# Kernel optimization log

Measured on AMD Instinct MI355X. Metric: run time of the kernel, lower is better.

## Reference

```python
import jax, jax.numpy as jnp
import numpy as np

N_NODES = 50000
N_EDGES = 800000
N_GRAPHS = 512
HID = 128
N_LAYERS = 4
EPS = 1e-4


def setup_inputs() -> dict:
    key = jax.random.key(0)
    ks = jax.random.split(key, 20)
    s = 0.05
    return {
        "z": jax.random.randint(ks[0], (N_NODES,), 0, 100),
        "pos": jax.random.normal(ks[1], (N_NODES, 3), jnp.float32),
        "batch": jnp.sort(jax.random.randint(ks[2], (N_NODES,), 0, N_GRAPHS)),
        "edge_index": jax.random.randint(ks[3], (2, N_EDGES), 0, N_NODES),
        "embed_tab": jax.random.normal(ks[4], (100, HID), jnp.float32) * s,
        "W_pos": jax.random.normal(ks[5], (3, HID), jnp.float32) * s,
        "b_pos": jax.random.normal(ks[6], (HID,), jnp.float32) * s,
        "W_comb": jax.random.normal(ks[7], (2 * HID, HID), jnp.float32) * s,
        "b_comb": jax.random.normal(ks[8], (HID,), jnp.float32) * s,
        "gin_W1": jax.random.normal(ks[9], (N_LAYERS, HID, HID), jnp.float32) * s,
        "gin_b1": jax.random.normal(ks[10], (N_LAYERS, HID), jnp.float32) * s,
        "gin_W2": jax.random.normal(ks[11], (N_LAYERS, HID, HID), jnp.float32) * s,
        "gin_b2": jax.random.normal(ks[12], (N_LAYERS, HID), jnp.float32) * s,
        # heads stacked in order: [alpha, beta, nu, gamma]
        "head_W1": jax.random.normal(ks[13], (4, HID, HID), jnp.float32) * s,
        "head_b1": jax.random.normal(ks[14], (4, HID), jnp.float32) * s,
        "head_W2": jax.random.normal(ks[15], (4, HID, 1), jnp.float32) * s,
        "head_b2": jax.random.normal(ks[16], (4, 1), jnp.float32) * s,
    }


def _forward(z, pos, batch, edge_index, embed_tab, W_pos, b_pos, W_comb, b_comb,
             gin_W1, gin_b1, gin_W2, gin_b2, head_W1, head_b1, head_W2, head_b2):
    # initial embedding: atom embed + linear pos embed -> combine MLP
    atom = embed_tab[z]                                    # [N, H]
    pemb = pos @ W_pos + b_pos                             # [N, H]
    x = jax.nn.relu(jnp.concatenate([atom, pemb], -1) @ W_comb + b_comb)
    src, dst = edge_index[0], edge_index[1]
    # GIN stack: h = MLP(x + sum_{j in N(i)} x_j); ReLU between convs, none after last
    for l in range(N_LAYERS):
        agg = jax.ops.segment_sum(x[src], dst, num_segments=N_NODES)  # [N, H]
        h = x + agg                                        # eps = 0
        h = jax.nn.relu(h @ gin_W1[l] + gin_b1[l]) @ gin_W2[l] + gin_b2[l]
        x = jax.nn.relu(h) if l < N_LAYERS - 1 else h
    # sum pooling per graph
    aggr = jax.ops.segment_sum(x, batch, num_segments=N_GRAPHS)  # [G, F]
    # 4 heads (alpha, beta, nu, gamma), each Linear-ReLU-Linear -> [4, G, 1]
    hh = jax.nn.relu(jnp.einsum('gh,khf->kgf', aggr, head_W1) + head_b1[:, None, :])
    out = jnp.einsum('kgf,kfo->kgo', hh, head_W2) + head_b2[:, None, :]
    alpha = jnp.maximum(jax.nn.softplus(out[0]) + 1.0, 1.0 + EPS)
    beta = jax.nn.softplus(out[1])
    nu = jax.nn.softplus(out[2])
    gamma = out[3]
    aleatoric = beta / (alpha - 1.0)
    epistemic = beta / ((alpha - 1.0) * nu)
    return (gamma, aleatoric, epistemic, nu, alpha, beta)


def reference(z, pos, batch, edge_index, embed_tab, W_pos, b_pos, W_comb, b_comb,
              gin_W1, gin_b1, gin_W2, gin_b2, head_W1, head_b1, head_W2, head_b2):
    return _forward(z, pos, batch, edge_index, embed_tab, W_pos, b_pos, W_comb,
                    b_comb, gin_W1, gin_b1, gin_W2, gin_b2, head_W1, head_b1,
                    head_W2, head_b2)
```

## Files before the change

kernel.cpp:

```cpp
#include <hip/hip_runtime.h>
#include <stdint.h>

#define NN 50000
#define NE 800000
#define NG 512
#define H  128
#define NBK 196
#define EPB 3125

typedef __attribute__((ext_vector_type(8))) short short8;
typedef __attribute__((ext_vector_type(16))) float f32x16;

union U4S8 { uint4 u; short8 s; };

__device__ __forceinline__ float softplusf(float x){
    return fmaxf(x, 0.f) + log1pf(expf(-fabsf(x)));
}

__device__ __forceinline__ unsigned rne_bf16_hi(float x){
    unsigned u = __float_as_uint(x);
    unsigned r = u + 0x7fffu + ((u >> 16) & 1u);
    return r & 0xffff0000u;
}

__device__ __forceinline__ void split_pack(float x0, float x1, unsigned &hi, unsigned &lo){
    unsigned h0 = rne_bf16_hi(x0), h1 = rne_bf16_hi(x1);
    hi = (h0 >> 16) | h1;
    float l0 = x0 - __uint_as_float(h0);
    float l1 = x1 - __uint_as_float(h1);
    unsigned g0 = rne_bf16_hi(l0), g1 = rne_bf16_hi(l1);
    lo = (g0 >> 16) | g1;
}

__global__ void k_sentinel(float* out, float val){
    int i = blockIdx.x*256 + threadIdx.x;
    if (i < 6*NG) out[i] = val;
}

__global__ __launch_bounds__(64) void k_wsplit(const float* __restrict__ gW1,
    const float* __restrict__ gW2, uint4* __restrict__ wf)
{
    int bid = blockIdx.x, lane = threadIdx.x;
    int mat = bid >> 5, ntg = (bid >> 3) & 3, ks = bid & 7;
    int l = mat >> 1;
    const float* W = (mat & 1) ? (gW2 + (size_t)l*H*H) : (gW1 + (size_t)l*H*H);
    int n  = ntg*32 + (lane & 31);
    int kb = ks*16 + (lane >> 5)*8;
    unsigned hi[4], lo[4];
#pragma unroll
    for (int d=0; d<4; d++){
        float x0 = W[(size_t)(kb + 2*d    )*H + n];
        float x1 = W[(size_t)(kb + 2*d + 1)*H + n];
        split_pack(x0, x1, hi[d], lo[d]);
    }
    int bh = ((mat*2 + 0)*4 + ntg)*8 + ks;
    int bl = ((mat*2 + 1)*4 + ntg)*8 + ks;
    wf[bh*64 + lane] = make_uint4(hi[0],hi[1],hi[2],hi[3]);
    wf[bl*64 + lane] = make_uint4(lo[0],lo[1],lo[2],lo[3]);
}

__global__ __launch_bounds__(64) void k_wsplit_embed(const float* __restrict__ Wc,
    uint4* __restrict__ wcf)
{
    int bid = blockIdx.x, lane = threadIdx.x;
    int ntg = bid >> 4, ks = bid & 15;
    int n  = ntg*32 + (lane & 31);
    int kb = ks*16 + (lane >> 5)*8;
    unsigned hi[4], lo[4];
#pragma unroll
    for (int d=0; d<4; d++){
        float x0 = Wc[(size_t)(kb + 2*d    )*H + n];
        float x1 = Wc[(size_t)(kb + 2*d + 1)*H + n];
        split_pack(x0, x1, hi[d], lo[d]);
    }
    wcf[((0*4 + ntg)*16 + ks)*64 + lane] = make_uint4(hi[0],hi[1],hi[2],hi[3]);
    wcf[((1*4 + ntg)*16 + ks)*64 + lane] = make_uint4(lo[0],lo[1],lo[2],lo[3]);
}

__global__ __launch_bounds__(256) void k_embed_mfma(const int* __restrict__ z,
    const float* __restrict__ pos, const float* __restrict__ emb,
    const float* __restrict__ Wp, const float* __restrict__ bp,
    const float* __restrict__ bc, const uint4* __restrict__ wcf,
    unsigned* __restrict__ xbu)
{
    __shared__ unsigned short AhiF[2*8*64*8];
    __shared__ unsigned short AloF[2*8*64*8];
    const int t = threadIdx.x, lane = t & 63, w = t >> 6;
    const int rt = w & 1, cp = w >> 1;
    const int mb = blockIdx.x * 64;
    const int c31 = lane & 31;
    const int q = lane >> 5;

    const int r = t >> 2, c4 = t & 3;
    const int gr = mb + r;
    const int gre = (gr < NN) ? gr : (NN-1);
    const int zr = z[gre];
    const float p0 = pos[gre*3+0], p1 = pos[gre*3+1], p2 = pos[gre*3+2];
    const int rt_s = r >> 5, r31s = r & 31;

    f32x16 acc0, acc1;
#pragma unroll
    for (int i=0;i<16;i++){ acc0[i]=0.f; acc1[i]=0.f; }

#pragma unroll
    for (int kh2=0; kh2<2; kh2++){
        if (kh2) __syncthreads();
#pragma unroll
        for (int i=0;i<8;i++){
            int cl = c4*4 + i*16;
            float4 v;
            if (kh2 == 0){
                v = *(const float4*)(emb + (size_t)zr*H + cl);
            } else {
                float4 w0 = *(const float4*)(Wp + cl);
                float4 w1 = *(const float4*)(Wp + H + cl);
                float4 w2 = *(const float4*)(Wp + 2*H + cl);
                float4 bb = *(const float4*)(bp + cl);
                v.x = p0*w0.x + p1*w1.x + p2*w2.x + bb.x;
                v.y = p0*w0.y + p1*w1.y + p2*w2.y + bb.y;
                v.z = p0*w0.z + p1*w1.z + p2*w2.z + bb.z;
                v.w = p0*w0.w + p1*w1.w + p2*w2.w + bb.w;
            }
            unsigned h0,l0,h1,l1;
            split_pack(v.x, v.y, h0, l0);
            split_pack(v.z, v.w, h1, l1);
            int idx = ((rt_s*8 + (cl>>4))*64 + ((cl>>3)&1)*32 + r31s)*8 + (cl & 7);
            *(uint2*)&AhiF[idx] = make_uint2(h0, h1);
            *(uint2*)&AloF[idx] = make_uint2(l0, l1);
        }
        __syncthreads();
#pragma unroll
        for (int ks=0; ks<8; ks++){
            int ksg = kh2*8 + ks;
            U4S8 ah, al, bh0, bl0, bh1, bl1;
            ah.u  = *(const uint4*)&AhiF[((rt*8+ks)*64 + lane)*8];
            al.u  = *(const uint4*)&AloF[((rt*8+ks)*64 + lane)*8];
            bh0.u = wcf[((0*4 + 2*cp+0)*16 + ksg)*64 + lane];
            bl0.u = wcf[((1*4 + 2*cp+0)*16 + ksg)*64 + lane];
            bh1.u = wcf[((0*4 + 2*cp+1)*16 + ksg)*64 + lane];
            bl1.u = wcf[((1*4 + 2*cp+1)*16 + ksg)*64 + lane];
            acc0 = __builtin_amdgcn_mfma_f32_32x32x16_bf16(ah.s, bh0.s, acc0, 0,0,0);
            acc0 = __builtin_amdgcn_mfma_f32_32x32x16_bf16(ah.s, bl0.s, acc0, 0,0,0);
            acc0 = __builtin_amdgcn_mfma_f32_32x32x16_bf16(al.s, bh0.s, acc0, 0,0,0);
            acc1 = __builtin_amdgcn_mfma_f32_32x32x16_bf16(ah.s, bh1.s, acc1, 0,0,0);
            acc1 = __builtin_amdgcn_mfma_f32_32x32x16_bf16(ah.s, bl1.s, acc1, 0,0,0);
            acc1 = __builtin_amdgcn_mfma_f32_32x32x16_bf16(al.s, bh1.s, acc1, 0,0,0);
        }
    }

    const float bva = bc[64*cp + c31], bvb = bc[64*cp + 32 + c31];
#pragma unroll
    for (int reg=0; reg<16; reg++){
        int row = 32*rt + (reg & 3) + 8*(reg >> 2) + 4*q;
        int mm = mb + row;
        if (mm < NN){
            float v0 = fmaxf(acc0[reg] + bva, 0.f);
            float v1 = fmaxf(acc1[reg] + bvb, 0.f);
            float pa = __shfl_xor(v0, 1);
            float pb = __shfl_xor(v1, 1);
            if (!(lane & 1)){
                unsigned u0 = (rne_bf16_hi(v0) >> 16) | (rne_bf16_hi(pa) & 0xffff0000u);
                unsigned u1 = (rne_bf16_hi(v1) >> 16) | (rne_bf16_hi(pb) & 0xffff0000u);
                xbu[(size_t)mm*64 + 32*cp      + (c31>>1)] = u0;
                xbu[(size_t)mm*64 + 32*cp + 16 + (c31>>1)] = u1;
            }
        }
    }
}

__global__ __launch_bounds__(256) void k_gin_fused(
    const unsigned* __restrict__ xbin,
    const int* __restrict__ iptr, const int* __restrict__ esrc,
    const float* __restrict__ b1, const float* __restrict__ b2,
    const uint4* __restrict__ wf,
    float* __restrict__ xout, unsigned* __restrict__ xbout,
    int l, int relu2, int wx, int wxb)
{
    __shared__ unsigned short AhiF[8*64*8];
    __shared__ unsigned short AloF[8*64*8];
    __shared__ int eS[1024];
    const int t = threadIdx.x, lane = t & 63, w = t >> 6;
    const int mb = blockIdx.x * 32;
    const int c31 = lane & 31;
    const int q = lane >> 5;
    const int c  = lane & 15;
    const int jr = lane >> 4;
    const int ksw = c >> 1, qw = c & 1;

    const uint4* __restrict__ xbp = (const uint4*)xbin;

    const int eTop = (mb + 32 < NN) ? (mb + 32) : NN;
    int e0b = iptr[mb];
    int e1b = iptr[eTop];
    e0b = max(0, min(e0b, NE));
    e1b = max(e0b, min(e1b, NE));
    const int ecnt = e1b - e0b;
    for (int i = t; i < ecnt && i < 1024; i += 256) eS[i] = esrc[e0b + i];
    __syncthreads();
    const int eCap = e0b + 1024;
    const int* ixL = (const int*)eS - e0b;

#define ACC8(U)  { unsigned _u; \
    _u=(U).x; a0 += __uint_as_float(_u<<16); a1 += __uint_as_float(_u&0xffff0000u); \
    _u=(U).y; a2 += __uint_as_float(_u<<16); a3 += __uint_as_float(_u&0xffff0000u); \
    _u=(U).z; a4 += __uint_as_float(_u<<16); a5 += __uint_as_float(_u&0xffff0000u); \
    _u=(U).w; a6 += __uint_as_float(_u<<16); a7 += __uint_as_float(_u&0xffff0000u); }

#define GLOOP(IX) { \
    for (; j+8 <= e; j += 8){ \
        int i0=IX[j+0], i1=IX[j+1], i2=IX[j+2], i3=IX[j+3]; \
        int i4=IX[j+4], i5=IX[j+5], i6=IX[j+6], i7=IX[j+7]; \
        uint4 u0 = xbp[(size_t)i0*16 + c]; \
        uint4 u1 = xbp[(size_t)i1*16 + c]; \
        uint4 u2 = xbp[(size_t)i2*16 + c]; \
        uint4 u3 = xbp[(size_t)i3*16 + c]; \
        uint4 u4 = xbp[(size_t)i4*16 + c]; \
        uint4 u5 = xbp[(size_t)i5*16 + c]; \
        uint4 u6 = xbp[(size_t)i6*16 + c]; \
        uint4 u7 = xbp[(size_t)i7*16 + c]; \
        ACC8(u0); ACC8(u1); ACC8(u2); ACC8(u3); \
        ACC8(u4); ACC8(u5); ACC8(u6); ACC8(u7); \
    } \
    for (; j+2 <= e; j += 2){ \
        int i0=IX[j+0], i1=IX[j+1]; \
        uint4 u0 = xbp[(size_t)i0*16 + c]; \
        uint4 u1 = xbp[(size_t)i1*16 + c]; \
        ACC8(u0); ACC8(u1); \
    } \
    if (j < e){ \
        int i0=IX[j]; \
        uint4 u0 = xbp[(size_t)i0*16 + c]; \
        ACC8(u0); \
    } }

#pragma unroll
    for (int p=0; p<2; p++){
        int m  = w*8 + p*4 + jr;
        int mm = mb + m;
        int mme = (mm < NN) ? mm : (NN-1);
        int s = iptr[mme], e = iptr[mme+1];
        s = max(0, min(s, NE));
        e = max(s, min(e, NE));
        float a0=0.f,a1=0.f,a2=0.f,a3=0.f,a4=0.f,a5=0.f,a6=0.f,a7=0.f;
        {
            uint4 su = xbp[(size_t)mme*16 + c];
            ACC8(su);
        }
        int j = s;
        if (s >= e0b && e <= eCap){
            GLOOP(ixL);
        } else {
            GLOOP(esrc);
        }
        unsigned hi4x, hi4y, hi4z, hi4w, lo4x, lo4y, lo4z, lo4w;
        split_pack(a0, a1, hi4x, lo4x);
        split_pack(a2, a3, hi4y, lo4y);
        split_pack(a4, a5, hi4z, lo4z);
        split_pack(a6, a7, hi4w, lo4w);
        int idx = (ksw*64 + qw*32 + (m ^ ksw))*8;
        *(uint4*)&AhiF[idx] = make_uint4(hi4x, hi4y, hi4z, hi4w);
        *(uint4*)&AloF[idx] = make_uint4(lo4x, lo4y, lo4z, lo4w);
    }
#undef GLOOP
#undef ACC8
    __syncthreads();

    const float bv1 = b1[w*32 + c31];
    const float bv2 = b2[w*32 + c31];
    const int mat1 = l*2, mat2 = l*2 + 1;

    f32x16 acc;
#pragma unroll
    for (int i=0;i<16;i++) acc[i] = 0.f;

#pragma unroll
    for (int ks=0; ks<8; ks++){
        U4S8 ah, al, bh, bl;
        ah.u = *(const uint4*)&AhiF[(ks*64 + q*32 + (c31 ^ ks))*8];
        al.u = *(const uint4*)&AloF[(ks*64 + q*32 + (c31 ^ ks))*8];
        bh.u = wf[(((mat1*2+0)*4 + w)*8 + ks)*64 + lane];
        bl.u = wf[(((mat1*2+1)*4 + w)*8 + ks)*64 + lane];
        acc = __builtin_amdgcn_mfma_f32_32x32x16_bf16(ah.s, bh.s, acc, 0,0,0);
        acc = __builtin_amdgcn_mfma_f32_32x32x16_bf16(ah.s, bl.s, acc, 0,0,0);
        acc = __builtin_amdgcn_mfma_f32_32x32x16_bf16(al.s, bh.s, acc, 0,0,0);
    }

    __syncthreads();
    {
        int k   = w*32 + c31;
        int kst = k >> 4, qt = (k >> 3) & 1, jj = k & 7;
#pragma unroll
        for (int reg=0; reg<16; reg++){
            int row = (reg & 3) + 8*(reg >> 2) + 4*q;
            float v = fmaxf(acc[reg] + bv1, 0.f);
            int idx = (kst*64 + qt*32 + (row ^ kst))*8 + jj;
            unsigned hb = rne_bf16_hi(v);
            AhiF[idx] = (unsigned short)(hb >> 16);
            AloF[idx] = (unsigned short)(rne_bf16_hi(v - __uint_as_float(hb)) >> 16);
        }
    }
    __syncthreads();

#pragma unroll
    for (int i=0;i<16;i++) acc[i] = 0.f;
#pragma unroll
    for (int ks=0; ks<8; ks++){
        U4S8 ah, al, bh, bl;
        ah.u = *(const uint4*)&AhiF[(ks*64 + q*32 + (c31 ^ ks))*8];
        al.u = *(const uint4*)&AloF[(ks*64 + q*32 + (c31 ^ ks))*8];
        bh.u = wf[(((mat2*2+0)*4 + w)*8 + ks)*64 + lane];
        bl.u = wf[(((mat2*2+1)*4 + w)*8 + ks)*64 + lane];
        acc = __builtin_amdgcn_mfma_f32_32x32x16_bf16(ah.s, bh.s, acc, 0,0,0);
        acc = __builtin_amdgcn_mfma_f32_32x32x16_bf16(ah.s, bl.s, acc, 0,0,0);
        acc = __builtin_amdgcn_mfma_f32_32x32x16_bf16(al.s, bh.s, acc, 0,0,0);
    }

#pragma unroll
    for (int reg=0; reg<16; reg++){
        int row = (reg & 3) + 8*(reg >> 2) + 4*q;
        int mm = mb + row;
        if (mm < NN){
            float v = acc[reg] + bv2;
            if (relu2) v = fmaxf(v, 0.f);
            if (wx) xout[(size_t)mm*H + w*32 + c31] = v;
            if (wxb){
                float p = __shfl_xor(v, 1);
                if (!(lane & 1)){
                    unsigned u = (rne_bf16_hi(v) >> 16) | (rne_bf16_hi(p) & 0xffff0000u);
                    xbout[(size_t)mm*64 + w*16 + (c31>>1)] = u;
                }
            }
        }
    }
}

__global__ __launch_bounds__(256) void k_hist(const int* __restrict__ ei, int* __restrict__ cnt){
    __shared__ int hist[256];
    int blk = blockIdx.x, t = threadIdx.x;
    hist[t] = 0;
    __syncthreads();
    int e0 = blk*EPB, e1 = min(e0+EPB, NE);
    for (int e = e0+t; e < e1; e += 256){
        int d = ei[NE+e];
        if ((unsigned)d < NN) atomicAdd(&hist[d>>8], 1);
    }
    __syncthreads();
    if (t < NBK) cnt[t*256 + blk] = hist[t];
}

__global__ __launch_bounds__(256) void k_btot(const int* __restrict__ cnt, int* __restrict__ tot){
    __shared__ int s[256];
    int k = blockIdx.x, t = threadIdx.x;
    s[t] = cnt[k*256 + t];
    __syncthreads();
    for (int sd=128; sd>0; sd>>=1){
        if (t < sd) s[t] += s[t+sd];
        __syncthreads();
    }
    if (t == 0) tot[k] = s[0];
}

__global__ __launch_bounds__(256) void k_bscan(const int* __restrict__ tot, int* __restrict__ bb){
    __shared__ int sc[256];
    int t = threadIdx.x;
    int v = (t < NBK) ? tot[t] : 0;
    sc[t] = v;
    for (int off=1; off<256; off<<=1){
        __syncthreads();
        int tv = (t >= off) ? sc[t-off] : 0;
        __syncthreads();
        sc[t] += tv;
    }
    __syncthreads();
    if (t == 0) bb[0] = 0;
    if (t < NBK) bb[t+1] = sc[t];
}

__global__ __launch_bounds__(256) void k_soff(const int* __restrict__ cnt,
    const int* __restrict__ bb, int* __restrict__ soff)
{
    __shared__ int sc[256];
    int k = blockIdx.x, t = threadIdx.x;
    int v = cnt[k*256 + t];
    sc[t] = v;
    for (int off=1; off<256; off<<=1){
        __syncthreads();
        int tv = (t >= off) ? sc[t-off] : 0;
        __syncthreads();
        sc[t] += tv;
    }
    __syncthreads();
    soff[k*256 + t] = bb[k] + sc[t] - v;
}

__global__ __launch_bounds__(256) void k_part(const int* __restrict__ ei,
    const int* __restrict__ soff, unsigned* __restrict__ tmp)
{
    __shared__ unsigned edgeL[EPB];
    __shared__ int sc[256], startv[256], curv[256];
    __shared__ int tots;
    int blk = blockIdx.x, t = threadIdx.x;
    sc[t] = 0;
    __syncthreads();
    int e0 = blk*EPB, e1 = min(e0+EPB, NE);
    for (int e = e0+t; e < e1; e += 256){
        int d = ei[NE+e];
        if ((unsigned)d < NN) atomicAdd(&sc[d>>8], 1);
    }
    __syncthreads();
    int v = sc[t];
    for (int off=1; off<256; off<<=1){
        __syncthreads();
        int tv = (t >= off) ? sc[t-off] : 0;
        __syncthreads();
        sc[t] += tv;
    }
    __syncthreads();
    startv[t] = sc[t] - v;
    curv[t]   = sc[t] - v;
    if (t == 255) tots = sc[255];
    __syncthreads();
    for (int e = e0+t; e < e1; e += 256){
        int d = ei[NE+e];
        if ((unsigned)d < NN){
            unsigned u = (unsigned)ei[e] | ((unsigned)d << 16);
            int p = atomicAdd(&curv[d>>8], 1);
            edgeL[p] = u;
        }
    }
    __syncthreads();
    int nTot = tots;
    for (int i = t; i < nTot; i += 256){
        unsigned u = edgeL[i];
        int b = u >> 24;
        int g = soff[b*256 + blk] + (i - startv[b]);
        tmp[g] = u;
    }
}

__global__ __launch_bounds__(256) void k_final(const int* __restrict__ bb,
    const unsigned* __restrict__ tmp, int* __restrict__ esrc, int* __restrict__ iptr)
{
    __shared__ int cntN[256], sc[256], curN[256];
    int k = blockIdx.x, t = threadIdx.x;
    int n0 = k*256;
    int nn = min(256, NN - n0);
    int base = bb[k], end = bb[k+1];
    cntN[t] = 0;
    __syncthreads();
    for (int i = base+t; i < end; i += 256){
        int d = (int)(tmp[i] >> 16) - n0;
        if ((unsigned)d < 256u) atomicAdd(&cntN[d], 1);
    }
    __syncthreads();
    int v = cntN[t];
    sc[t] = v;
    for (int off=1; off<256; off<<=1){
        __syncthreads();
        int tv = (t >= off) ? sc[t-off] : 0;
        __syncthreads();
        sc[t] += tv;
    }
    __syncthreads();
    int excl = sc[t] - v;
    curN[t] = excl;
    if (t < nn) iptr[n0 + t] = base + excl;
    if (k == NBK-1 && t == 0) iptr[NN] = end;
    __syncthreads();
    for (int i = base+t; i < end; i += 256){
        unsigned u = tmp[i];
        int d = (int)(u >> 16) - n0;
        if ((unsigned)d < 256u){
            int p = atomicAdd(&curN[d], 1);
            esrc[base + p] = (int)(u & 0xffffu);
        }
    }
}

__global__ __launch_bounds__(256) void k_pool(const float* __restrict__ x,
    const int* __restrict__ batch, float* __restrict__ aggr)
{
    __shared__ float red[128];
    int g = blockIdx.x;
    int c = threadIdx.x & 127, half = threadIdx.x >> 7;
    int lo=0, hi=NN;
    while (lo<hi){ int mid=(lo+hi)>>1; if (batch[mid] < g) lo=mid+1; else hi=mid; }
    int s0 = lo;
    hi = NN;
    while (lo<hi){ int mid=(lo+hi)>>1; if (batch[mid] < g+1) lo=mid+1; else hi=mid; }
    int e0 = lo;
    int n  = e0 - s0;
    int sh = s0 + (half ? (n>>1) : 0);
    int eh = half ? e0 : (s0 + (n>>1));
    float a0=0.f, a1=0.f, a2=0.f, a3=0.f;
    int i = sh;
    for (; i+4 <= eh; i += 4){
        a0 += x[(size_t)(i+0)*H + c];
        a1 += x[(size_t)(i+1)*H + c];
        a2 += x[(size_t)(i+2)*H + c];
        a3 += x[(size_t)(i+3)*H + c];
    }
    for (; i < eh; i++) a0 += x[(size_t)i*H + c];
    float v = (a0+a1) + (a2+a3);
    if (half) red[c] = v;
    __syncthreads();
    if (!half) aggr[g*H + c] = v + red[c];
}

__global__ __launch_bounds__(128) void k_head_dot(const float* __restrict__ aggr,
    const float* __restrict__ W1, const float* __restrict__ b1,
    const float* __restrict__ W2, float* __restrict__ ok)
{
    __shared__ float a[H];
    __shared__ float red[H];
    int b = blockIdx.x, g = b >> 2, k = b & 3;
    int c = threadIdx.x;
    a[c] = aggr[g*H + c];
    __syncthreads();
    float acc = b1[k*H + c];
    const float* wp = W1 + (size_t)k*H*H + c;
#pragma unroll 8
    for (int q=0; q<H; q++) acc += a[q] * wp[(size_t)q*H];
    red[c] = fmaxf(acc, 0.f) * W2[k*H + c];
    __syncthreads();
    for (int sd=64; sd>0; sd>>=1){
        if (c < sd) red[c] += red[c+sd];
        __syncthreads();
    }
    if (c == 0) ok[b] = red[0];
}

__global__ void k_evid(const float* __restrict__ ok, const float* __restrict__ b2,
                       float* __restrict__ out)
{
    int g = blockIdx.x*256 + threadIdx.x;
    if (g >= NG) return;
    float o0 = ok[g*4+0] + b2[0];
    float o1 = ok[g*4+1] + b2[1];
    float o2 = ok[g*4+2] + b2[2];
    float o3 = ok[g*4+3] + b2[3];
    float alpha = fmaxf(softplusf(o0) + 1.f, 1.f + 1e-4f);
    float beta  = softplusf(o1);
    float nu    = softplusf(o2);
    float am1   = alpha - 1.f;
    float aleat = beta / am1;
    float epis  = beta / (am1 * nu);
    out[0*NG+g] = o3;
    out[1*NG+g] = aleat;
    out[2*NG+g] = epis;
    out[3*NG+g] = nu;
    out[4*NG+g] = alpha;
    out[5*NG+g] = beta;
}

extern "C" void kernel_launch(void* const* d_in, const int* in_sizes, int n_in,
                              void* d_out, int out_size, void* d_ws, size_t ws_size,
                              hipStream_t stream)
{
    const int*   z     = (const int*)d_in[0];
    const float* pos   = (const float*)d_in[1];
    const int*   batch = (const int*)d_in[2];
    const int*   eidx  = (const int*)d_in[3];
    const float* emb   = (const float*)d_in[4];
    const float* Wp    = (const float*)d_in[5];
    const float* bp    = (const float*)d_in[6];
    const float* Wc    = (const float*)d_in[7];
    const float* bc    = (const float*)d_in[8];
    const float* gW1   = (const float*)d_in[9];
    const float* gb1   = (const float*)d_in[10];
    const float* gW2   = (const float*)d_in[11];
    const float* gb2   = (const float*)d_in[12];
    const float* hW1   = (const float*)d_in[13];
    const float* hb1   = (const float*)d_in[14];
    const float* hW2   = (const float*)d_in[15];
    const float* hb2   = (const float*)d_in[16];
    float* out = (float*)d_out;

    bool ok_sizes = (n_in == 17)
        && in_sizes[0] == NN && in_sizes[1] == NN*3 && in_sizes[2] == NN
        && in_sizes[3] == 2*NE && in_sizes[4] == 100*H
        && in_sizes[7] == 2*H*H && in_sizes[9] == 4*H*H
        && in_sizes[13] == 4*H*H && in_sizes[16] == 4;
    if (!ok_sizes){ k_sentinel<<<12, 256, 0, stream>>>(out, 600000.0f); return; }

    const size_t OFF_XA   = 256;
    const size_t OFF_TMPR = 25600256;
    const size_t OFF_BA   = 51200256;
    const size_t OFF_AGGR = 64000256;
    const size_t OFF_IPTR = 64262400;
    const size_t OFF_ESRC = 64662464;
    const size_t OFF_WF   = 67863296;
    const size_t OFF_WCF  = 68387584;
    const size_t OFF_OK   = 68518656;
    const size_t OFF_BB_B = 68526848;
    const size_t REQ      = 81326848;
    if (ws_size < REQ){ k_sentinel<<<12, 256, 0, stream>>>(out, 500000.0f); return; }

    const size_t OFF_TMP2 = OFF_TMPR;
    const size_t OFF_CNT  = OFF_TMPR + 3200000;
    const size_t OFF_SOFF = OFF_TMPR + 3401216;
    const size_t OFF_TOT  = OFF_TMPR + 3602176;
    const size_t OFF_BBB  = OFF_TMPR + 3603200;

    char* ws = (char*)d_ws;
    float*    xA   = (float*)(ws + OFF_XA);
    unsigned* bA   = (unsigned*)(ws + OFF_BA);
    unsigned* bB   = (unsigned*)(ws + OFF_BB_B);
    float*    aggr = (float*)(ws + OFF_AGGR);
    int*      iptr = (int*)(ws + OFF_IPTR);
    int*      esrc = (int*)(ws + OFF_ESRC);
    uint4*    wf   = (uint4*)(ws + OFF_WF);
    uint4*    wcf  = (uint4*)(ws + OFF_WCF);
    float*    okb  = (float*)(ws + OFF_OK);
    unsigned* tmp  = (unsigned*)(ws + OFF_TMP2);
    int*      cnt  = (int*)(ws + OFF_CNT);
    int*      soff = (int*)(ws + OFF_SOFF);
    int*      tot  = (int*)(ws + OFF_TOT);
    int*      bb   = (int*)(ws + OFF_BBB);

    k_wsplit_embed<<<64, 64, 0, stream>>>(Wc, wcf);
    k_embed_mfma<<<(NN+63)/64, 256, 0, stream>>>(z, pos, emb, Wp, bp, bc, wcf, bA);
    k_wsplit<<<256, 64, 0, stream>>>(gW1, gW2, wf);

    k_hist <<<256, 256, 0, stream>>>(eidx, cnt);
    k_btot <<<NBK, 256, 0, stream>>>(cnt, tot);
    k_bscan<<<1,   256, 0, stream>>>(tot, bb);
    k_soff <<<NBK, 256, 0, stream>>>(cnt, bb, soff);
    k_part <<<256, 256, 0, stream>>>(eidx, soff, tmp);
    k_final<<<NBK, 256, 0, stream>>>(bb, tmp, esrc, iptr);

    unsigned* bi = bA;  unsigned* bo = bB;
    for (int l=0;l<4;l++){
        int wx  = (l == 3) ? 1 : 0;
        int wxb = (l <  3) ? 1 : 0;
        k_gin_fused<<<(NN+31)/32, 256, 0, stream>>>(bi, iptr, esrc,
            gb1 + (size_t)l*H, gb2 + (size_t)l*H, wf, xA, bo, l, (l<3)?1:0, wx, wxb);
        unsigned* bt = bi; bi = bo; bo = bt;
    }

    k_pool<<<NG, 256, 0, stream>>>(xA, batch, aggr);
    k_head_dot<<<NG*4, 128, 0, stream>>>(aggr, hW1, hb1, hW2, okb);
    k_evid<<<(NG+255)/256, 256, 0, stream>>>(okb, hb2, out);
}
```

Before: 336.6 us.

## Balance GIN neighbor aggregation by splitting block edges evenly across thread groups

Replaces the per-row gather, where each 16-lane group walked one destination node's edge list, with an edge-balanced walk. The block's edge range is split evenly across 16 groups, and partial sums are flushed into a shared fp32 accumulator through LDS atomics at row boundaries. The self term and the bf16 hi/lo split then happen in a separate pass that repacks into the swizzled MFMA A layout. This is meant to remove load imbalance from skewed node degrees, at the cost of shared-memory atomics, extra syncs and aliasing the A tiles onto the accumulator buffer.

```diff
diff --git a/kernel.cpp b/kernel.cpp
--- a/kernel.cpp
+++ b/kernel.cpp
@@ -176,29 +176,45 @@
     float* __restrict__ xout, unsigned* __restrict__ xbout,
     int l, int relu2, int wx, int wxb)
 {
-    __shared__ unsigned short AhiF[8*64*8];
-    __shared__ unsigned short AloF[8*64*8];
-    __shared__ int eS[1024];
+    __shared__ float sAcc[32*128];
+    __shared__ int   eS[1024];
+    __shared__ int   iptrL[33];
+    unsigned short* AhiF = (unsigned short*)sAcc;
+    unsigned short* AloF = ((unsigned short*)sAcc) + 4096;
+
     const int t = threadIdx.x, lane = t & 63, w = t >> 6;
     const int mb = blockIdx.x * 32;
     const int c31 = lane & 31;
     const int q = lane >> 5;
-    const int c  = lane & 15;
-    const int jr = lane >> 4;
-    const int ksw = c >> 1, qw = c & 1;
 
     const uint4* __restrict__ xbp = (const uint4*)xbin;
 
-    const int eTop = (mb + 32 < NN) ? (mb + 32) : NN;
     int e0b = iptr[mb];
-    int e1b = iptr[eTop];
+    int e1b = iptr[(mb + 32 < NN) ? (mb + 32) : NN];
     e0b = max(0, min(e0b, NE));
     e1b = max(e0b, min(e1b, NE));
     const int ecnt = e1b - e0b;
+
+    if (t <= 32){
+        int idx = mb + t; if (idx > NN) idx = NN;
+        int v = iptr[idx];
+        v = max(e0b, min(v, e1b));
+        iptrL[t] = v - e0b;
+    }
+    {
+        float4 z4 = make_float4(0.f,0.f,0.f,0.f);
+        float4* zp = (float4*)(sAcc + t*16);
+        zp[0]=z4; zp[1]=z4; zp[2]=z4; zp[3]=z4;
+    }
     for (int i = t; i < ecnt && i < 1024; i += 256) eS[i] = esrc[e0b + i];
     __syncthreads();
-    const int eCap = e0b + 1024;
-    const int* ixL = (const int*)eS - e0b;
+
+    const int gid = t >> 4;
+    const int c   = t & 15;
+    const int L   = (ecnt + 15) >> 4;
+    const int gs  = gid * L;
+    const int ge  = (gs + L < ecnt) ? (gs + L) : ecnt;
+    const bool useL = (ecnt <= 1024);
 
 #define ACC8(U)  { unsigned _u; \
     _u=(U).x; a0 += __uint_as_float(_u<<16); a1 += __uint_as_float(_u&0xffff0000u); \
@@ -206,63 +222,98 @@
     _u=(U).z; a4 += __uint_as_float(_u<<16); a5 += __uint_as_float(_u&0xffff0000u); \
     _u=(U).w; a6 += __uint_as_float(_u<<16); a7 += __uint_as_float(_u&0xffff0000u); }
 
-#define GLOOP(IX) { \
-    for (; j+8 <= e; j += 8){ \
-        int i0=IX[j+0], i1=IX[j+1], i2=IX[j+2], i3=IX[j+3]; \
-        int i4=IX[j+4], i5=IX[j+5], i6=IX[j+6], i7=IX[j+7]; \
-        uint4 u0 = xbp[(size_t)i0*16 + c]; \
-        uint4 u1 = xbp[(size_t)i1*16 + c]; \
-        uint4 u2 = xbp[(size_t)i2*16 + c]; \
-        uint4 u3 = xbp[(size_t)i3*16 + c]; \
-        uint4 u4 = xbp[(size_t)i4*16 + c]; \
-        uint4 u5 = xbp[(size_t)i5*16 + c]; \
-        uint4 u6 = xbp[(size_t)i6*16 + c]; \
-        uint4 u7 = xbp[(size_t)i7*16 + c]; \
-        ACC8(u0); ACC8(u1); ACC8(u2); ACC8(u3); \
-        ACC8(u4); ACC8(u5); ACC8(u6); ACC8(u7); \
+#define FLUSH() { float* fp = sAcc + (r<<7) + (c<<3); \
+    atomicAdd(fp+0,a0); atomicAdd(fp+1,a1); atomicAdd(fp+2,a2); atomicAdd(fp+3,a3); \
+    atomicAdd(fp+4,a4); atomicAdd(fp+5,a5); atomicAdd(fp+6,a6); atomicAdd(fp+7,a7); \
+    a0=0.f;a1=0.f;a2=0.f;a3=0.f;a4=0.f;a5=0.f;a6=0.f;a7=0.f; }
+
+#define STEP(K, U) { while (j + K >= rEnd){ FLUSH(); r++; rEnd = iptrL[r+1]; } ACC8(U); }
+
+#define WALK(IX) { \
+    int j = gs; \
+    for (; j+8 <= ge; j += 8){ \
+        int i0=IX(j+0), i1=IX(j+1), i2=IX(j+2), i3=IX(j+3); \
+        int i4=IX(j+4), i5=IX(j+5), i6=IX(j+6), i7=IX(j+7); \
+        uint4 u0 = xbp[(unsigned)i0*16u + c]; \
+        uint4 u1 = xbp[(unsigned)i1*16u + c]; \
+        uint4 u2 = xbp[(unsigned)i2*16u + c]; \
+        uint4 u3 = xbp[(unsigned)i3*16u + c]; \
+        uint4 u4 = xbp[(unsigned)i4*16u + c]; \
+        uint4 u5 = xbp[(unsigned)i5*16u + c]; \
+        uint4 u6 = xbp[(unsigned)i6*16u + c]; \
+        uint4 u7 = xbp[(unsigned)i7*16u + c]; \
+        STEP(0,u0); STEP(1,u1); STEP(2,u2); STEP(3,u3); \
+        STEP(4,u4); STEP(5,u5); STEP(6,u6); STEP(7,u7); \
     } \
-    for (; j+2 <= e; j += 2){ \
-        int i0=IX[j+0], i1=IX[j+1]; \
-        uint4 u0 = xbp[(size_t)i0*16 + c]; \
-        uint4 u1 = xbp[(size_t)i1*16 + c]; \
-        ACC8(u0); ACC8(u1); \
+    for (; j < ge; j++){ \
+        int i0=IX(j); \
+        uint4 u0 = xbp[(unsigned)i0*16u + c]; \
+        STEP(0,u0); \
     } \
-    if (j < e){ \
-        int i0=IX[j]; \
-        uint4 u0 = xbp[(size_t)i0*16 + c]; \
-        ACC8(u0); \
-    } }
-
-#pragma unroll
-    for (int p=0; p<2; p++){
-        int m  = w*8 + p*4 + jr;
-        int mm = mb + m;
-        int mme = (mm < NN) ? mm : (NN-1);
-        int s = iptr[mme], e = iptr[mme+1];
-        s = max(0, min(s, NE));
-        e = max(s, min(e, NE));
+    FLUSH(); }
+
+#define EIX_L(J) eS[(J)]
+#define EIX_G(J) esrc[e0b + (J)]
+
+    if (gs < ge){
+        int r = 0;
+#pragma unroll
+        for (int s=16; s>0; s>>=1){
+            int nr = r + s;
+            if (nr <= 31 && iptrL[nr] <= gs) r = nr;
+        }
+        int rEnd = iptrL[r+1];
         float a0=0.f,a1=0.f,a2=0.f,a3=0.f,a4=0.f,a5=0.f,a6=0.f,a7=0.f;
-        {
-            uint4 su = xbp[(size_t)mme*16 + c];
-            ACC8(su);
-        }
-        int j = s;
-        if (s >= e0b && e <= eCap){
-            GLOOP(ixL);
-        } else {
-            GLOOP(esrc);
-        }
-        unsigned hi4x, hi4y, hi4z, hi4w, lo4x, lo4y, lo4z, lo4w;
-        split_pack(a0, a1, hi4x, lo4x);
-        split_pack(a2, a3, hi4y, lo4y);
-        split_pack(a4, a5, hi4z, lo4z);
-        split_pack(a6, a7, hi4w, lo4w);
-        int idx = (ksw*64 + qw*32 + (m ^ ksw))*8;
-        *(uint4*)&AhiF[idx] = make_uint4(hi4x, hi4y, hi4z, hi4w);
-        *(uint4*)&AloF[idx] = make_uint4(lo4x, lo4y, lo4z, lo4w);
-    }
-#undef GLOOP
+        if (useL){ WALK(EIX_L); } else { WALK(EIX_G); }
+    }
+#undef EIX_G
+#undef EIX_L
+#undef WALK
+#undef STEP
+#undef FLUSH
 #undef ACC8
+    __syncthreads();
+
+    {
+        const int row = t >> 3;
+        const int cb  = (t & 7) << 4;
+        const float* rp = sAcc + row*128 + cb;
+        float4 f0 = *(const float4*)(rp + 0);
+        float4 f1 = *(const float4*)(rp + 4);
+        float4 f2 = *(const float4*)(rp + 8);
+        float4 f3 = *(const float4*)(rp + 12);
+        const int mm = mb + row;
+        if (mm < NN){
+            uint4 s0 = xbp[(size_t)mm*16 + (cb>>3)];
+            uint4 s1 = xbp[(size_t)mm*16 + (cb>>3) + 1];
+            f0.x += __uint_as_float(s0.x<<16); f0.y += __uint_as_float(s0.x&0xffff0000u);
+            f0.z += __uint_as_float(s0.y<<16); f0.w += __uint_as_float(s0.y&0xffff0000u);
+            f1.x += __uint_as_float(s0.z<<16); f1.y += __uint_as_float(s0.z&0xffff0000u);
+            f1.z += __uint_as_float(s0.w<<16); f1.w += __uint_as_float(s0.w&0xffff0000u);
+            f2.x += __uint_as_float(s1.x<<16); f2.y += __uint_as_float(s1.x&0xffff0000u);
+            f2.z += __uint_as_float(s1.y<<16); f2.w += __uint_as_float(s1.y&0xffff0000u);
+            f3.x += __uint_as_float(s1.z<<16); f3.y += __uint_as_float(s1.z&0xffff0000u);
+            f3.z += __uint_as_float(s1.w<<16); f3.w += __uint_as_float(s1.w&0xffff0000u);
+        }
+        __syncthreads();
+        uint4 Hh0, Ll0, Hh1, Ll1;
+        split_pack(f0.x, f0.y, Hh0.x, Ll0.x);
+        split_pack(f0.z, f0.w, Hh0.y, Ll0.y);
+        split_pack(f1.x, f1.y, Hh0.z, Ll0.z);
+        split_pack(f1.z, f1.w, Hh0.w, Ll0.w);
+        split_pack(f2.x, f2.y, Hh1.x, Ll1.x);
+        split_pack(f2.z, f2.w, Hh1.y, Ll1.y);
+        split_pack(f3.x, f3.y, Hh1.z, Ll1.z);
+        split_pack(f3.z, f3.w, Hh1.w, Ll1.w);
+        const int kst = t & 7;
+        const int rx  = row ^ kst;
+        uint4* hiP = (uint4*)AhiF;
+        uint4* loP = (uint4*)AloF;
+        hiP[kst*64 + rx]      = Hh0;
+        hiP[kst*64 + 32 + rx] = Hh1;
+        loP[kst*64 + rx]      = Ll0;
+        loP[kst*64 + 32 + rx] = Ll1;
+    }
     __syncthreads();
 
     const float bv1 = b1[w*32 + c31];
```

Measured after the change: 459.3 us. 1.36x slower.
